# Kernel optimization log

Hardware: AMD Instinct MI355X
Metric: run time of the kernel (lower is better)

## Reference

```python
import jax, jax.numpy as jnp
import numpy as np

H = 1024
T = 50000
WASHOUT = 200
SPECTRAL_RADIUS = 0.9


def setup_inputs() -> dict:
    key = jax.random.key(0)
    k_u, k_in, k_res, k_mask = jax.random.split(key, 4)
    u = jax.random.normal(k_u, (T,), dtype=jnp.float32)
    # w_in ~ Uniform(-0.5, 0.5), density 1.0, input_scaling 1.0
    w_in = jax.random.uniform(k_in, (H,), dtype=jnp.float32) - 0.5
    # w_res ~ Uniform(-0.5, 0.5), density 1.0, scaled to spectral radius 0.9
    w_res = np.asarray(jax.random.uniform(k_res, (H, H), dtype=jnp.float32)) - 0.5
    rho = float(np.max(np.abs(np.linalg.eigvals(w_res.astype(np.float64)))))
    w_res = jnp.asarray((SPECTRAL_RADIUS / rho) * w_res, dtype=jnp.float32)
    # readout weights (inference path uses the buffer, initialized to ones)
    w_out = jnp.ones((H,), dtype=jnp.float32)
    # w_out_density = 1.0 -> mask is a random permutation of all H indices
    w_out_mask = jax.random.permutation(k_mask, H).astype(jnp.int64)
    return {"u": u, "w_in": w_in, "w_res": w_res, "w_out": w_out,
            "w_out_mask": w_out_mask}


def reference(u, w_in, w_res, w_out, w_out_mask):
    # Echo-state recurrence: x_t = tanh(w_in * u_t + w_res @ x_{t-1})
    # Inference path (y=None, awgn_test_std=0, adc_quantization=None).
    def step(x, u_t):
        x_new = jnp.tanh(w_in * u_t + w_res @ x)  # [H]
        return x_new, x_new[w_out_mask]           # emit masked state

    x0 = jnp.zeros((H,), dtype=u.dtype)
    _, X = jax.lax.scan(step, x0, u)              # X: [T, H]
    return X[WASHOUT:] @ w_out                    # [T - WASHOUT]
```

## Files before the change

kernel.cpp:

```cpp
#include <hip/hip_runtime.h>


#define HH    1024
#define TT    50000
#define WASH  200
#define NROLE 128
#define NBLK  2048
#define NT    64
#define SPIN_CAP (1u << 20)

typedef unsigned int u32;
typedef u32 u32x4 __attribute__((ext_vector_type(4)));
typedef float f32x4 __attribute__((ext_vector_type(4)));
typedef float f32x2 __attribute__((ext_vector_type(2)));

__device__ __forceinline__ float fast_tanh(float x) {
  float e = __builtin_amdgcn_exp2f(x * 2.8853900817779268f);
  return fmaf(-2.0f, __builtin_amdgcn_rcpf(e + 1.0f), 1.0f);
}

template <int CTRL>
__device__ __forceinline__ float dpp_movf(float x) {
  return __int_as_float(__builtin_amdgcn_update_dpp(
      0, __float_as_int(x), CTRL, 0xF, 0xF, true));
}
__device__ __forceinline__ float swz_xor16(float x) {
  return __int_as_float(__builtin_amdgcn_ds_swizzle(__float_as_int(x), 0x401F));
}

#define YREDUCE()                                                         \
  { y += __shfl_xor(y, 32);                                               \
    y += swz_xor16(y);                                                    \
    y += dpp_movf<0x128>(y);                             \
    y += dpp_movf<0x141>(y);                             \
    y += dpp_movf<0x1B>(y);                              \
    y += dpp_movf<0xB1>(y); }

#define POLL_ISSUE(b)                                                                 \
  asm volatile("global_load_dwordx4 %0, %1, off sc1"             : "=v"(p0) : "v"(b)); \
  asm volatile("global_load_dwordx4 %0, %1, off offset:1024 sc1" : "=v"(p1) : "v"(b)); \
  asm volatile("global_load_dwordx4 %0, %1, off offset:2048 sc1" : "=v"(p2) : "v"(b)); \
  asm volatile("global_load_dwordx4 %0, %1, off offset:3072 sc1" : "=v"(p3) : "v"(b))

#define POLL_WAIT0()                                                      \
  asm volatile("s_waitcnt vmcnt(0)"                                       \
               : "+v"(p0), "+v"(p1), "+v"(p2), "+v"(p3))

#define TAGBAD(p) ((p.x ^ want) | (p.y ^ want) | (p.z ^ want) | (p.w ^ want))
#define TAGBAD_ALL ((TAGBAD(p0) | TAGBAD(p1) | TAGBAD(p2) | TAGBAD(p3)) & 0xFFu)

#define UNPACK2(p, b2)                                                    \
  { xv2[b2+0] = (f32x2){__uint_as_float(p.x & 0xFFFFFF00u),               \
                        __uint_as_float(p.y & 0xFFFFFF00u)};              \
    xv2[b2+1] = (f32x2){__uint_as_float(p.z & 0xFFFFFF00u),               \
                        __uint_as_float(p.w & 0xFFFFFF00u)}; }

#define DECLW(r) f32x2 W##r##0, W##r##1, W##r##2, W##r##3,                \
                      W##r##4, W##r##5, W##r##6, W##r##7

#define LOADW(r) do {                                                     \
  const float* wp = w_res + (size_t)(8 * w + r) * HH + 4 * l;             \
  f32x4 va = *(const f32x4*)(wp);                                         \
  f32x4 vb = *(const f32x4*)(wp + 256);                                   \
  f32x4 vc = *(const f32x4*)(wp + 512);                                   \
  f32x4 vd = *(const f32x4*)(wp + 768);                                   \
  W##r##0 = (f32x2){va.x, va.y}; W##r##1 = (f32x2){va.z, va.w};           \
  W##r##2 = (f32x2){vb.x, vb.y}; W##r##3 = (f32x2){vb.z, vb.w};           \
  W##r##4 = (f32x2){vc.x, vc.y}; W##r##5 = (f32x2){vc.z, vc.w};           \
  W##r##6 = (f32x2){vd.x, vd.y}; W##r##7 = (f32x2){vd.z, vd.w};           \
} while (0)

#define FMAR(r) do {                                                      \
  acc2[r] = __builtin_elementwise_fma(W##r##0, xv2[0], acc2[r]);          \
  acc2[r] = __builtin_elementwise_fma(W##r##1, xv2[1], acc2[r]);          \
  acc2[r] = __builtin_elementwise_fma(W##r##2, xv2[2], acc2[r]);          \
  acc2[r] = __builtin_elementwise_fma(W##r##3, xv2[3], acc2[r]);          \
  acc2[r] = __builtin_elementwise_fma(W##r##4, xv2[4], acc2[r]);          \
  acc2[r] = __builtin_elementwise_fma(W##r##5, xv2[5], acc2[r]);          \
  acc2[r] = __builtin_elementwise_fma(W##r##6, xv2[6], acc2[r]);          \
  acc2[r] = __builtin_elementwise_fma(W##r##7, xv2[7], acc2[r]);          \
} while (0)

__global__ __launch_bounds__(NT, 1) void esn_kernel(
    const float* __restrict__ u,
    const float* __restrict__ w_in,
    const float* __restrict__ w_res,
    const float* __restrict__ w_out,
    const int*   __restrict__ mask,
    float*       __restrict__ out,
    char*        __restrict__ ws)
{
  const int l = threadIdx.x;

  u32 xcc;
  asm("s_getreg_b32 %0, hwreg(HW_REG_XCC_ID)" : "=s"(xcc));
  if (xcc != 0) return;
  int slot = 0;
  if (l == 0) slot = atomicAdd((int*)ws, 1);
  slot = __shfl(slot, 0);
  if (slot >= NROLE) return;
  const int w = slot;

  u32* xb0 = (u32*)(ws + 4096);
  u32* xb1 = xb0 + HH;

  __shared__ float lds_c[HH];
  for (int h = l; h < HH; h += NT) lds_c[mask[h]] = w_out[h];
  __syncthreads();

  DECLW(0); DECLW(1); DECLW(2); DECLW(3);
  DECLW(4); DECLW(5); DECLW(6); DECLW(7);
  LOADW(0); LOADW(1); LOADW(2); LOADW(3);
  LOADW(4); LOADW(5); LOADW(6); LOADW(7);

  const float win = w_in[8 * w + (l >> 3)];

  f32x2 cr2[8];
#pragma unroll
  for (int k = 0; k < 4; ++k) {
    f32x4 v = *(const f32x4*)(lds_c + 256 * k + 4 * l);
    cr2[2*k+0] = (f32x2){v.x, v.y};
    cr2[2*k+1] = (f32x2){v.z, v.w};
  }

  const u32* pA0 = xb0 + 4 * l;
  const u32* pA1 = xb1 + 4 * l;
  const int drow = 8 * w + (l >> 3);
  u32* d0 = xb0 + drow;
  u32* d1 = xb1 + drow;

  u32x4 p0, p1, p2, p3;
  const int lb32 = l & 32, lb16 = l & 16, lb8 = l & 8;
  int dead = 0;

  for (int t = 0; t < TT; ++t) {
    const int pa = t & 1;
    const float u_t = u[t];
    f32x2 acc2[8];
#pragma unroll
    for (int i = 0; i < 8; ++i) acc2[i] = (f32x2){0.f, 0.f};
    f32x2 xv2[8];
    const bool doRead = ((t & 127) == w) && (t > 0);

    if (t > 0 && !dead) {
      if (((t - 1) & 127) == w) __builtin_amdgcn_s_sleep(1);
      else                      __builtin_amdgcn_s_sleep(3);

      const u32* b = pa ? pA0 : pA1;
      const u32 want = (u32)t & 0xFFu;
      u32 guard = 0;
      for (;;) {
        POLL_ISSUE(b);
        POLL_WAIT0();
        if (!TAGBAD_ALL) break;
        if (++guard > SPIN_CAP) { dead = 1; break; }
      }
      UNPACK2(p0, 0); UNPACK2(p1, 2); UNPACK2(p2, 4); UNPACK2(p3, 6);
      FMAR(0); FMAR(1); FMAR(2); FMAR(3);
      FMAR(4); FMAR(5); FMAR(6); FMAR(7);
    }

    const float a0 = acc2[0].x + acc2[0].y, a1 = acc2[1].x + acc2[1].y;
    const float a2 = acc2[2].x + acc2[2].y, a3 = acc2[3].x + acc2[3].y;
    const float a4 = acc2[4].x + acc2[4].y, a5 = acc2[5].x + acc2[5].y;
    const float a6 = acc2[6].x + acc2[6].y, a7 = acc2[7].x + acc2[7].y;
    float t0 = (lb32 ? a4 : a0) + __shfl_xor(lb32 ? a0 : a4, 32);
    float t1 = (lb32 ? a5 : a1) + __shfl_xor(lb32 ? a1 : a5, 32);
    float t2 = (lb32 ? a6 : a2) + __shfl_xor(lb32 ? a2 : a6, 32);
    float t3 = (lb32 ? a7 : a3) + __shfl_xor(lb32 ? a3 : a7, 32);
    float s0 = (lb16 ? t2 : t0) + swz_xor16(lb16 ? t0 : t2);
    float s1 = (lb16 ? t3 : t1) + swz_xor16(lb16 ? t1 : t3);
    float r0 = (lb8 ? s1 : s0) + dpp_movf<0x128>(lb8 ? s0 : s1);
    r0 += dpp_movf<0x141>(r0);
    r0 += dpp_movf<0x1B>(r0);
    r0 += dpp_movf<0xB1>(r0);

    float x_new = fast_tanh(fmaf(win, u_t, r0));
    u32 packed = ((__float_as_uint(x_new) + 0x80u) & 0xFFFFFF00u)
               | ((u32)(t + 1) & 0xFFu);
    if ((l & 7) == 0) {
      u32* dst = pa ? d1 : d0;
      asm volatile("global_store_dword %0, %1, off" :: "v"(dst), "v"(packed));
    }

    if (doRead) {
      f32x2 y2 = (f32x2){0.f, 0.f};
#pragma unroll
      for (int jj = 0; jj < 8; ++jj)
        y2 = __builtin_elementwise_fma(cr2[jj], xv2[jj], y2);
      float y = y2.x + y2.y;
      YREDUCE();
      if (l == 0 && t - 1 >= WASH) out[t - 1 - WASH] = y;
    }
  }

  if (w == 0) {
    const u32 want = (u32)TT & 0xFFu;
    u32 guard = 0;
    for (;;) {
      POLL_ISSUE(pA1);
      POLL_WAIT0();
      if (!TAGBAD_ALL) break;
      if (++guard > SPIN_CAP) break;
    }
    f32x2 xv2[8];
    UNPACK2(p0, 0); UNPACK2(p1, 2); UNPACK2(p2, 4); UNPACK2(p3, 6);
    f32x2 y2 = (f32x2){0.f, 0.f};
#pragma unroll
    for (int jj = 0; jj < 8; ++jj)
      y2 = __builtin_elementwise_fma(cr2[jj], xv2[jj], y2);
    float y = y2.x + y2.y;
    YREDUCE();
    if (l == 0) out[TT - 1 - WASH] = y;
  }
}

extern "C" void kernel_launch(void* const* d_in, const int* in_sizes, int n_in,
                              void* d_out, int out_size, void* d_ws, size_t ws_size,
                              hipStream_t stream) {
  const float* u     = (const float*)d_in[0];
  const float* w_in  = (const float*)d_in[1];
  const float* w_res = (const float*)d_in[2];
  const float* w_out = (const float*)d_in[3];
  const int*   mask  = (const int*)d_in[4];
  float* out = (float*)d_out;

  hipMemsetAsync(d_ws, 0, 64, stream);

  esn_kernel<<<NBLK, NT, 0, stream>>>(u, w_in, w_res, w_out, mask, out,
                                      (char*)d_ws);
}
```

Baseline: 50.44 ms.

## Group four wave roles per block and share polled state through LDS

Moves from 128 single-wave blocks to 32 blocks of four waves each. Every wave now polls only a quarter of the global state vector and writes it to LDS, and a block barrier shares the full vector. This cuts the global polling traffic per wave by four. In exchange it adds a __syncthreads on the serial critical path of each timestep.

```diff
diff --git a/kernel.cpp b/kernel.cpp
--- a/kernel.cpp
+++ b/kernel.cpp
@@ -4,9 +4,9 @@
 #define HH    1024
 #define TT    50000
 #define WASH  200
-#define NROLE 128
-#define NBLK  2048
-#define NT    64
+#define NBROLE 32
+#define NBLK  512
+#define NT    256
 #define SPIN_CAP (1u << 20)
 
 typedef unsigned int u32;
@@ -36,30 +36,24 @@
     y += dpp_movf<0x1B>(y);                              \
     y += dpp_movf<0xB1>(y); }
 
-#define POLL_ISSUE(b)                                                                 \
-  asm volatile("global_load_dwordx4 %0, %1, off sc1"             : "=v"(p0) : "v"(b)); \
-  asm volatile("global_load_dwordx4 %0, %1, off offset:1024 sc1" : "=v"(p1) : "v"(b)); \
-  asm volatile("global_load_dwordx4 %0, %1, off offset:2048 sc1" : "=v"(p2) : "v"(b)); \
-  asm volatile("global_load_dwordx4 %0, %1, off offset:3072 sc1" : "=v"(p3) : "v"(b))
-
-#define POLL_WAIT0()                                                      \
-  asm volatile("s_waitcnt vmcnt(0)"                                       \
-               : "+v"(p0), "+v"(p1), "+v"(p2), "+v"(p3))
-
-#define TAGBAD(p) ((p.x ^ want) | (p.y ^ want) | (p.z ^ want) | (p.w ^ want))
-#define TAGBAD_ALL ((TAGBAD(p0) | TAGBAD(p1) | TAGBAD(p2) | TAGBAD(p3)) & 0xFFu)
-
-#define UNPACK2(p, b2)                                                    \
-  { xv2[b2+0] = (f32x2){__uint_as_float(p.x & 0xFFFFFF00u),               \
-                        __uint_as_float(p.y & 0xFFFFFF00u)};              \
-    xv2[b2+1] = (f32x2){__uint_as_float(p.z & 0xFFFFFF00u),               \
-                        __uint_as_float(p.w & 0xFFFFFF00u)}; }
+#define POLL_ISSUE1(b)                                                    \
+  asm volatile("global_load_dwordx4 %0, %1, off sc1" : "=v"(p) : "v"(b))
+#define POLL_WAIT1()                                                      \
+  asm volatile("s_waitcnt vmcnt(0)" : "+v"(p))
+
+#define TAGBAD(q) ((((q.x ^ want) | (q.y ^ want) | (q.z ^ want) | (q.w ^ want)) & 0xFFu))
+
+#define UNPACK2(q, b2)                                                    \
+  { xv2[b2+0] = (f32x2){__uint_as_float(q.x & 0xFFFFFF00u),               \
+                        __uint_as_float(q.y & 0xFFFFFF00u)};              \
+    xv2[b2+1] = (f32x2){__uint_as_float(q.z & 0xFFFFFF00u),               \
+                        __uint_as_float(q.w & 0xFFFFFF00u)}; }
 
 #define DECLW(r) f32x2 W##r##0, W##r##1, W##r##2, W##r##3,                \
                       W##r##4, W##r##5, W##r##6, W##r##7
 
 #define LOADW(r) do {                                                     \
-  const float* wp = w_res + (size_t)(8 * w + r) * HH + 4 * l;             \
+  const float* wp = w_res + (size_t)(32 * b + 8 * ww + r) * HH + 4 * l;   \
   f32x4 va = *(const f32x4*)(wp);                                         \
   f32x4 vb = *(const f32x4*)(wp + 256);                                   \
   f32x4 vc = *(const f32x4*)(wp + 512);                                   \
@@ -90,30 +84,33 @@
     float*       __restrict__ out,
     char*        __restrict__ ws)
 {
-  const int l = threadIdx.x;
+  const int tid = threadIdx.x;
+  const int l  = tid & 63;
+  const int ww = tid >> 6;
 
   u32 xcc;
   asm("s_getreg_b32 %0, hwreg(HW_REG_XCC_ID)" : "=s"(xcc));
   if (xcc != 0) return;
-  int slot = 0;
-  if (l == 0) slot = atomicAdd((int*)ws, 1);
-  slot = __shfl(slot, 0);
-  if (slot >= NROLE) return;
-  const int w = slot;
+
+  __shared__ int slot_s;
+  __shared__ float lds_c[HH];
+  __shared__ u32 lds_x[2][HH];
+
+  if (tid == 0) slot_s = atomicAdd((int*)ws, 1);
+  for (int h = tid; h < HH; h += NT) lds_c[mask[h]] = w_out[h];
+  __syncthreads();
+  const int b = slot_s;
+  if (b >= NBROLE) return;
 
   u32* xb0 = (u32*)(ws + 4096);
   u32* xb1 = xb0 + HH;
-
-  __shared__ float lds_c[HH];
-  for (int h = l; h < HH; h += NT) lds_c[mask[h]] = w_out[h];
-  __syncthreads();
 
   DECLW(0); DECLW(1); DECLW(2); DECLW(3);
   DECLW(4); DECLW(5); DECLW(6); DECLW(7);
   LOADW(0); LOADW(1); LOADW(2); LOADW(3);
   LOADW(4); LOADW(5); LOADW(6); LOADW(7);
 
-  const float win = w_in[8 * w + (l >> 3)];
+  const float win = w_in[32 * b + 8 * ww + (l >> 3)];
 
   f32x2 cr2[8];
 #pragma unroll
@@ -123,13 +120,15 @@
     cr2[2*k+1] = (f32x2){v.z, v.w};
   }
 
-  const u32* pA0 = xb0 + 4 * l;
-  const u32* pA1 = xb1 + 4 * l;
-  const int drow = 8 * w + (l >> 3);
+  const u32* pS0 = xb0 + 256 * ww + 4 * l;
+  const u32* pS1 = xb1 + 256 * ww + 4 * l;
+  const int drow = 32 * b + 8 * ww + (l >> 3);
   u32* d0 = xb0 + drow;
   u32* d1 = xb1 + drow;
-
-  u32x4 p0, p1, p2, p3;
+  const int stg = 256 * ww + 4 * l;
+
+  const int role = (b << 2) | ww;
+  u32x4 p;
   const int lb32 = l & 32, lb16 = l & 16, lb8 = l & 8;
   int dead = 0;
 
@@ -140,22 +139,30 @@
 #pragma unroll
     for (int i = 0; i < 8; ++i) acc2[i] = (f32x2){0.f, 0.f};
     f32x2 xv2[8];
-    const bool doRead = ((t & 127) == w) && (t > 0);
-
-    if (t > 0 && !dead) {
-      if (((t - 1) & 127) == w) __builtin_amdgcn_s_sleep(1);
-      else                      __builtin_amdgcn_s_sleep(3);
-
-      const u32* b = pa ? pA0 : pA1;
-      const u32 want = (u32)t & 0xFFu;
-      u32 guard = 0;
-      for (;;) {
-        POLL_ISSUE(b);
-        POLL_WAIT0();
-        if (!TAGBAD_ALL) break;
-        if (++guard > SPIN_CAP) { dead = 1; break; }
+    const bool doRead = ((t & 127) == role) && (t > 0);
+
+    if (t > 0) {
+      const int h = pa ^ 1;
+      if (!dead) {
+        __builtin_amdgcn_s_sleep(2);
+        const u32* src = h ? pS1 : pS0;
+        const u32 want = (u32)t & 0xFFu;
+        u32 guard = 0;
+        for (;;) {
+          POLL_ISSUE1(src);
+          POLL_WAIT1();
+          if (!TAGBAD(p)) break;
+          if (++guard > SPIN_CAP) { dead = 1; break; }
+        }
       }
-      UNPACK2(p0, 0); UNPACK2(p1, 2); UNPACK2(p2, 4); UNPACK2(p3, 6);
+      *(u32x4*)(&lds_x[h][stg]) = p;
+      __syncthreads();
+      u32x4 c0 = *(const u32x4*)(&lds_x[h][  0 + 4 * l]);
+      u32x4 c1 = *(const u32x4*)(&lds_x[h][256 + 4 * l]);
+      u32x4 c2 = *(const u32x4*)(&lds_x[h][512 + 4 * l]);
+      u32x4 c3 = *(const u32x4*)(&lds_x[h][768 + 4 * l]);
+      { const u32 want = 0; (void)want; }
+      UNPACK2(c0, 0); UNPACK2(c1, 2); UNPACK2(c2, 4); UNPACK2(c3, 6);
       FMAR(0); FMAR(1); FMAR(2); FMAR(3);
       FMAR(4); FMAR(5); FMAR(6); FMAR(7);
     }
@@ -194,24 +201,32 @@
     }
   }
 
-  if (w == 0) {
+  if (b == 0) {
     const u32 want = (u32)TT & 0xFFu;
     u32 guard = 0;
     for (;;) {
-      POLL_ISSUE(pA1);
-      POLL_WAIT0();
-      if (!TAGBAD_ALL) break;
+      POLL_ISSUE1(pS1);
+      POLL_WAIT1();
+      if (!TAGBAD(p)) break;
       if (++guard > SPIN_CAP) break;
     }
-    f32x2 xv2[8];
-    UNPACK2(p0, 0); UNPACK2(p1, 2); UNPACK2(p2, 4); UNPACK2(p3, 6);
-    f32x2 y2 = (f32x2){0.f, 0.f};
-#pragma unroll
-    for (int jj = 0; jj < 8; ++jj)
-      y2 = __builtin_elementwise_fma(cr2[jj], xv2[jj], y2);
-    float y = y2.x + y2.y;
-    YREDUCE();
-    if (l == 0) out[TT - 1 - WASH] = y;
+    *(u32x4*)(&lds_x[1][stg]) = p;
+    __syncthreads();
+    if (ww == 0) {
+      f32x2 xv2[8];
+      u32x4 c0 = *(const u32x4*)(&lds_x[1][  0 + 4 * l]);
+      u32x4 c1 = *(const u32x4*)(&lds_x[1][256 + 4 * l]);
+      u32x4 c2 = *(const u32x4*)(&lds_x[1][512 + 4 * l]);
+      u32x4 c3 = *(const u32x4*)(&lds_x[1][768 + 4 * l]);
+      UNPACK2(c0, 0); UNPACK2(c1, 2); UNPACK2(c2, 4); UNPACK2(c3, 6);
+      f32x2 y2 = (f32x2){0.f, 0.f};
+#pragma unroll
+      for (int jj = 0; jj < 8; ++jj)
+        y2 = __builtin_elementwise_fma(cr2[jj], xv2[jj], y2);
+      float y = y2.x + y2.y;
+      YREDUCE();
+      if (l == 0) out[TT - 1 - WASH] = y;
+    }
   }
 }
 
```

After: 47.97 ms. 1.05x faster.
